# Optimization experiments

Hardware: AMD Instinct MI355X
Metric: run time of the kernel (lower is better)

The kernel has to match this reference:

```python
import jax, jax.numpy as jnp
import numpy as np

B, T, D = 4, 2048, 1024

def setup_inputs() -> dict:
    key = jax.random.key(0)
    kx, kq, kk, kv = jax.random.split(key, 4)
    scale = 1.0 / np.sqrt(D)
    return {
        "x": jax.random.normal(kx, (B, T, D), dtype=jnp.float32),
        "Wq": jax.random.normal(kq, (D, D), dtype=jnp.float32) * scale,
        "Wk": jax.random.normal(kk, (D, D), dtype=jnp.float32) * scale,
        "Wv": jax.random.normal(kv, (D, D), dtype=jnp.float32) * scale,
    }

def reference(x, Wq, Wk, Wv):
    # torch Linear: y = x @ W.T (no bias, qkv_bias=False)
    q = jnp.einsum("btd,od->bto", x, Wq)
    k = jnp.einsum("btd,od->bto", x, Wk)
    v = jnp.einsum("btd,od->bto", x, Wv)
    scores = jnp.einsum("bqd,bkd->bqk", q, k)
    # NOTE: source uses non-in-place masked_fill whose result is discarded,
    # so NO causal mask is actually applied. Faithfully reproduced here.
    inv_sqrt_d = 1.0 / np.sqrt(k.shape[-1]).astype(np.float32)
    weights = jax.nn.softmax(scores * inv_sqrt_d, axis=-1)
    # dropout p=0.0 -> identity
    return jnp.einsum("bqk,bkd->bqd", weights, v)
```

## Files before the change

kernel.cpp:

```cpp
#include <hip/hip_runtime.h>
#include <hip/hip_bf16.h>
#include <hip/hip_fp16.h>
#include <type_traits>

typedef _Float16 f16;
typedef __attribute__((ext_vector_type(8))) _Float16 f16x8;
typedef __attribute__((ext_vector_type(4))) float floatx4;

#define B_ 4
#define T_ 2048
#define D_ 1024

#define XB_OFF   0ul
#define WB_OFF   16777216ul
#define QKV_OFF  23068672ul
#define S_OFF    73400320ul
#define VT_OFF   0ul

#define ASYNC16(gp, lp) \
    __builtin_amdgcn_global_load_lds((const __attribute__((address_space(1))) unsigned int*)(gp), \
                                     (__attribute__((address_space(3))) unsigned int*)(lp), 16, 0, 0)

template<int N> __device__ __forceinline__ void vmwait() {
    if constexpr (N == 0)      asm volatile("s_waitcnt vmcnt(0)" ::: "memory");
    else if constexpr (N == 4) asm volatile("s_waitcnt vmcnt(4)" ::: "memory");
    else if constexpr (N == 6) asm volatile("s_waitcnt vmcnt(6)" ::: "memory");
    else static_assert(N == 0, "unsupported vmcnt literal");
}

__global__ __launch_bounds__(256) void cast_all(
    const float* __restrict__ x, const float* __restrict__ wq,
    const float* __restrict__ wk, const float* __restrict__ wv,
    f16* __restrict__ xb, f16* __restrict__ wb)
{
    long i = (long)blockIdx.x * 256 + threadIdx.x;
    const float4* src; f16* dst;
    if (i < 2097152L)            { src = (const float4*)x;  dst = xb; }
    else if (i < 2359296L)       { i -= 2097152L; src = (const float4*)wq; dst = wb; }
    else if (i < 2621440L)       { i -= 2359296L; src = (const float4*)wk; dst = wb + 1048576; }
    else                         { i -= 2621440L; src = (const float4*)wv; dst = wb + 2097152; }
    float4 v = src[i];
    union { f16 h[4]; uint2 u; } o;
    o.h[0] = (f16)v.x; o.h[1] = (f16)v.y; o.h[2] = (f16)v.z; o.h[3] = (f16)v.w;
    ((uint2*)dst)[i] = o.u;
}

template <typename CT, int BN, int WN>
__global__ __launch_bounds__(256, 3) void gemm_nt(
    const f16* __restrict__ A, int lda, long sA,
    const f16* __restrict__ B, int ldb, long sB,
    CT* __restrict__ C, int ldc, long sC,
    int K, float alpha)
{
    __shared__ f16 As[3][128 * 32];
    __shared__ f16 Bs[3][BN * 32];
    constexpr int L = 2 + BN / 64;

    const int tid = threadIdx.x;
    const int m0 = blockIdx.y * 128;
    const int n0 = blockIdx.x * BN;
    const int bz = blockIdx.z;
    A += (long)bz * sA;
    B += (long)bz * sB;
    C += (long)bz * sC;

    const int w  = tid >> 6;
    const int l  = tid & 63;
    const int wm = (w >> 1) * 64;
    const int wn = (w & 1) * WN;
    const int lr = l & 15;
    const int kg = l >> 4;
    const int kx = kg ^ ((lr >> 1) & 3);

    constexpr int NI = WN / 16;
    floatx4 acc[4][NI] = {};

    const int srow = tid >> 2;
    const int gsl  = (tid & 3) ^ ((tid >> 3) & 3);
    const long ldaL = lda, ldbL = ldb;
    const f16* Aptr = A + (long)(m0 + srow) * ldaL + gsl * 8;
    const f16* Bptr = B + (long)(n0 + srow) * ldbL + gsl * 8;

    auto stage = [&](f16* Ad, f16* Bd, int kk) {
        #pragma unroll
        for (int rh = 0; rh < 2; rh++)
            ASYNC16(Aptr + kk + rh * 64 * ldaL, Ad + rh * 2048 + w * 512);
        #pragma unroll
        for (int rh = 0; rh < BN / 64; rh++)
            ASYNC16(Bptr + kk + rh * 64 * ldbL, Bd + rh * 2048 + w * 512);
    };

    f16 *a0 = As[0], *a1 = As[1], *a2 = As[2];
    f16 *b0 = Bs[0], *b1 = Bs[1], *b2 = Bs[2];

    const int NT = K >> 5;
    stage(a0, b0, 0);
    stage(a1, b1, 32);

    for (int t = 0; t < NT; ++t) {
        if (t < NT - 1) vmwait<L>(); else vmwait<0>();
        __builtin_amdgcn_s_barrier();
        __builtin_amdgcn_sched_barrier(0);

        if (t + 2 < NT) stage(a2, b2, (t + 2) << 5);

        f16x8 af[4], bf[NI];
        #pragma unroll
        for (int mi = 0; mi < 4; mi++)
            af[mi] = *(const f16x8*)&a0[(wm + mi * 16 + lr) * 32 + kx * 8];
        #pragma unroll
        for (int ni = 0; ni < NI; ni++)
            bf[ni] = *(const f16x8*)&b0[(wn + ni * 16 + lr) * 32 + kx * 8];
        #pragma unroll
        for (int mi = 0; mi < 4; mi++)
            #pragma unroll
            for (int ni = 0; ni < NI; ni++)
                acc[mi][ni] = __builtin_amdgcn_mfma_f32_16x16x32_f16(af[mi], bf[ni], acc[mi][ni], 0, 0, 0);

        f16* ta = a0; a0 = a1; a1 = a2; a2 = ta;
        f16* tb = b0; b0 = b1; b1 = b2; b2 = tb;
    }

    #pragma unroll
    for (int mi = 0; mi < 4; mi++) {
        #pragma unroll
        for (int ni = 0; ni < NI; ni++) {
            #pragma unroll
            for (int r = 0; r < 4; r++) {
                int row = m0 + wm + mi * 16 + kg * 4 + r;
                int col = n0 + wn + ni * 16 + lr;
                float v = acc[mi][ni][r] * alpha;
                if constexpr (std::is_same<CT, float>::value)
                    C[(long)row * ldc + col] = v;
                else
                    C[(long)row * ldc + col] = (f16)v;
            }
        }
    }
}

__global__ __launch_bounds__(256) void transpose_v(const f16* __restrict__ qkv, f16* __restrict__ vt)
{
    __shared__ f16 tile[32][33];
    int b  = blockIdx.z;
    int j0 = blockIdx.x * 32;
    int d0 = blockIdx.y * 32;
    int tx = threadIdx.x & 31;
    int ty = threadIdx.x >> 5;
    #pragma unroll
    for (int i = 0; i < 4; i++) {
        int j = j0 + ty + i * 8;
        tile[ty + i * 8][tx] = qkv[((long)b * T_ + j) * 3072 + 2048 + d0 + tx];
    }
    __syncthreads();
    #pragma unroll
    for (int i = 0; i < 4; i++) {
        int d = d0 + ty + i * 8;
        vt[((long)b * D_ + d) * T_ + j0 + tx] = tile[tx][ty + i * 8];
    }
}

__global__ __launch_bounds__(256) void softmax_rows(f16* __restrict__ S)
{
    long row = (long)blockIdx.x * 4 + (threadIdx.x >> 6);
    int l = threadIdx.x & 63;
    uint4* p4 = (uint4*)(S + row * 2048);
    union U { uint4 u; f16 h[8]; } d[4];
    float v[32];
    float mx = -1e30f;
    #pragma unroll
    for (int i = 0; i < 4; i++) {
        d[i].u = p4[i * 64 + l];
        #pragma unroll
        for (int j = 0; j < 8; j++) { v[i * 8 + j] = (float)d[i].h[j]; mx = fmaxf(mx, v[i * 8 + j]); }
    }
    #pragma unroll
    for (int off = 32; off; off >>= 1) mx = fmaxf(mx, __shfl_xor(mx, off, 64));
    float s = 0.f;
    #pragma unroll
    for (int i = 0; i < 32; i++) { v[i] = __expf(v[i] - mx); s += v[i]; }
    #pragma unroll
    for (int off = 32; off; off >>= 1) s += __shfl_xor(s, off, 64);
    float inv = 1.f / s;
    #pragma unroll
    for (int i = 0; i < 4; i++) {
        #pragma unroll
        for (int j = 0; j < 8; j++) d[i].h[j] = (f16)(v[i * 8 + j] * inv);
        p4[i * 64 + l] = d[i].u;
    }
}

extern "C" void kernel_launch(void* const* d_in, const int* in_sizes, int n_in,
                              void* d_out, int out_size, void* d_ws, size_t ws_size,
                              hipStream_t stream)
{
    const float* x  = (const float*)d_in[0];
    const float* wq = (const float*)d_in[1];
    const float* wk = (const float*)d_in[2];
    const float* wv = (const float*)d_in[3];
    float* out = (float*)d_out;
    char* ws = (char*)d_ws;
    f16* xb  = (f16*)(ws + XB_OFF);
    f16* wb  = (f16*)(ws + WB_OFF);
    f16* qkv = (f16*)(ws + QKV_OFF);
    f16* s   = (f16*)(ws + S_OFF);
    f16* vt  = (f16*)(ws + VT_OFF);

    cast_all<<<11264, 256, 0, stream>>>(x, wq, wk, wv, xb, wb);

    gemm_nt<f16, 128, 64><<<dim3(24, 64, 1), 256, 0, stream>>>(
        xb, 1024, 0L, wb, 1024, 0L, qkv, 3072, 0L, 1024, 1.0f);

    transpose_v<<<dim3(64, 32, 4), 256, 0, stream>>>(qkv, vt);

    gemm_nt<f16, 128, 64><<<dim3(16, 16, 4), 256, 0, stream>>>(
        qkv,        3072, (long)T_ * 3072,
        qkv + 1024, 3072, (long)T_ * 3072,
        s,          2048, (long)T_ * 2048, 1024, 0.03125f);

    softmax_rows<<<2048, 256, 0, stream>>>(s);

    gemm_nt<float, 128, 64><<<dim3(8, 16, 4), 256, 0, stream>>>(
        s,  2048, (long)T_ * 2048,
        vt, 2048, (long)D_ * 2048,
        out, 1024, (long)T_ * 1024, 2048, 1.0f);
}
```

Baseline: 286.1 us.

## Add 256x256-tile 8-wave GEMM with split-phase pipelining for QKV and scores

Adds a new GEMM kernel that uses 512 threads and 256x256 output tiles with a K-step of 64. It double-buffers in LDS and interleaves LDS fragment reads, async global-to-LDS loads, barriers and MFMA bursts raised with s_setprio, in the style of ping-pong scheduling. The QKV projection and the QK^T score GEMM now use this kernel, while the PV GEMM keeps the old one. The larger tiles should increase data reuse and overlap memory traffic with math. In exchange the kernel carries heavy register pressure (128 accumulator floats) and launches fewer blocks: 384 and 256 workgroups for 256 CUs, which risks load imbalance.

```diff
diff --git a/kernel.cpp b/kernel.cpp
--- a/kernel.cpp
+++ b/kernel.cpp
@@ -27,6 +27,7 @@
     else if constexpr (N == 6) asm volatile("s_waitcnt vmcnt(6)" ::: "memory");
     else static_assert(N == 0, "unsupported vmcnt literal");
 }
+#define BAR()  do { __builtin_amdgcn_s_barrier(); __builtin_amdgcn_sched_barrier(0); } while (0)
 
 __global__ __launch_bounds__(256) void cast_all(
     const float* __restrict__ x, const float* __restrict__ wq,
@@ -43,6 +44,154 @@
     union { f16 h[4]; uint2 u; } o;
     o.h[0] = (f16)v.x; o.h[1] = (f16)v.y; o.h[2] = (f16)v.z; o.h[3] = (f16)v.w;
     ((uint2*)dst)[i] = o.u;
+}
+
+template <typename CT>
+__global__ __launch_bounds__(512, 2) void gemm8_nt(
+    const f16* __restrict__ A, int lda, long sA,
+    const f16* __restrict__ B, int ldb, long sB,
+    CT* __restrict__ C, int ldc, long sC,
+    int K, float alpha)
+{
+    __shared__ f16 lds[2][32768];
+
+    const int tid = threadIdx.x;
+    const int m0 = blockIdx.y * 256;
+    const int n0 = blockIdx.x * 256;
+    const int bz = blockIdx.z;
+    A += (long)bz * sA; B += (long)bz * sB; C += (long)bz * sC;
+
+    const int w  = tid >> 6;
+    const int l  = tid & 63;
+    const int wm = w >> 2;
+    const int wn = w & 3;
+    const int lr = l & 15;
+    const int kg = l >> 4;
+    const int kx = kg ^ ((lr >> 1) & 3);
+
+    floatx4 acc[8][4] = {};
+
+    const int srow = tid >> 2;
+    const int gsl  = (tid & 3) ^ ((tid >> 3) & 3);
+    const long ldaL = lda, ldbL = ldb;
+    const f16* Ag = A + (long)(m0 + srow) * ldaL + gsl * 8;
+    const f16* Bg = B + (long)(n0 + srow) * ldbL + gsl * 8;
+
+    auto stA = [&](int buf, int h, int t) {
+        f16* d = &lds[buf][h * 8192 + w * 512];
+        const f16* g = Ag + (long)(h * 128) * ldaL + t * 64;
+        ASYNC16(g,      d);
+        ASYNC16(g + 32, d + 4096);
+    };
+    auto stB = [&](int buf, int h, int t) {
+        f16* d = &lds[buf][16384 + h * 8192 + w * 512];
+        const f16* g = Bg + (long)(h * 128) * ldbL + t * 64;
+        ASYNC16(g,      d);
+        ASYNC16(g + 32, d + 4096);
+    };
+
+    const int NT = K >> 6;
+    stA(0, 0, 0); stA(0, 1, 0); stB(0, 0, 0); stB(0, 1, 0);
+    stB(1, 0, 1); stB(1, 1, 1);
+    vmwait<4>();
+    BAR();
+
+    const int abase = wm * 8192;
+    const int bbase = 16384 + (wn >> 1) * 8192 + (wn & 1) * 2048;
+    f16x8 af[2][4], bf0[2][2], bf1[2][2];
+
+    for (int u = 0; u < NT; ++u) {
+        const int cur = u & 1;
+        const f16* Lc = lds[cur];
+
+        #pragma unroll
+        for (int kk = 0; kk < 2; kk++) {
+            #pragma unroll
+            for (int mi = 0; mi < 4; mi++)
+                af[kk][mi] = *(const f16x8*)&Lc[abase + kk * 4096 + (mi * 16 + lr) * 32 + kx * 8];
+            #pragma unroll
+            for (int ni = 0; ni < 2; ni++)
+                bf0[kk][ni] = *(const f16x8*)&Lc[bbase + kk * 4096 + (ni * 16 + lr) * 32 + kx * 8];
+        }
+        if (u + 1 < NT) stA(cur ^ 1, 0, u + 1);
+        BAR();
+        __builtin_amdgcn_s_setprio(1);
+        #pragma unroll
+        for (int kk = 0; kk < 2; kk++)
+            #pragma unroll
+            for (int mi = 0; mi < 4; mi++)
+                #pragma unroll
+                for (int ni = 0; ni < 2; ni++)
+                    acc[mi][ni] = __builtin_amdgcn_mfma_f32_16x16x32_f16(af[kk][mi], bf0[kk][ni], acc[mi][ni], 0, 0, 0);
+        __builtin_amdgcn_s_setprio(0);
+        BAR();
+
+        #pragma unroll
+        for (int kk = 0; kk < 2; kk++)
+            #pragma unroll
+            for (int ni = 0; ni < 2; ni++)
+                bf1[kk][ni] = *(const f16x8*)&Lc[bbase + kk * 4096 + ((ni + 2) * 16 + lr) * 32 + kx * 8];
+        if (u + 1 < NT) stA(cur ^ 1, 1, u + 1);
+        BAR();
+        __builtin_amdgcn_s_setprio(1);
+        #pragma unroll
+        for (int kk = 0; kk < 2; kk++)
+            #pragma unroll
+            for (int mi = 0; mi < 4; mi++)
+                #pragma unroll
+                for (int ni = 0; ni < 2; ni++)
+                    acc[mi][ni + 2] = __builtin_amdgcn_mfma_f32_16x16x32_f16(af[kk][mi], bf1[kk][ni], acc[mi][ni + 2], 0, 0, 0);
+        __builtin_amdgcn_s_setprio(0);
+        BAR();
+
+        #pragma unroll
+        for (int kk = 0; kk < 2; kk++)
+            #pragma unroll
+            for (int mi = 0; mi < 4; mi++)
+                af[kk][mi] = *(const f16x8*)&Lc[abase + kk * 4096 + ((mi + 4) * 16 + lr) * 32 + kx * 8];
+        if (u + 2 < NT) stB(cur, 0, u + 2);
+        BAR();
+        __builtin_amdgcn_s_setprio(1);
+        #pragma unroll
+        for (int kk = 0; kk < 2; kk++)
+            #pragma unroll
+            for (int mi = 0; mi < 4; mi++)
+                #pragma unroll
+                for (int ni = 0; ni < 2; ni++)
+                    acc[mi + 4][ni + 2] = __builtin_amdgcn_mfma_f32_16x16x32_f16(af[kk][mi], bf1[kk][ni], acc[mi + 4][ni + 2], 0, 0, 0);
+        __builtin_amdgcn_s_setprio(0);
+        BAR();
+
+        if (u + 2 < NT) stB(cur, 1, u + 2);
+        BAR();
+        __builtin_amdgcn_s_setprio(1);
+        #pragma unroll
+        for (int kk = 0; kk < 2; kk++)
+            #pragma unroll
+            for (int mi = 0; mi < 4; mi++)
+                #pragma unroll
+                for (int ni = 0; ni < 2; ni++)
+                    acc[mi + 4][ni] = __builtin_amdgcn_mfma_f32_16x16x32_f16(af[kk][mi], bf0[kk][ni], acc[mi + 4][ni], 0, 0, 0);
+        __builtin_amdgcn_s_setprio(0);
+        if (u + 2 < NT)      vmwait<4>();
+        else if (u + 1 < NT) vmwait<0>();
+        BAR();
+    }
+
+    #pragma unroll
+    for (int mi = 0; mi < 8; mi++)
+        #pragma unroll
+        for (int ni = 0; ni < 4; ni++)
+            #pragma unroll
+            for (int r = 0; r < 4; r++) {
+                int row = m0 + wm * 128 + mi * 16 + kg * 4 + r;
+                int col = n0 + wn * 64 + ni * 16 + lr;
+                float v = acc[mi][ni][r] * alpha;
+                if constexpr (std::is_same<CT, float>::value)
+                    C[(long)row * ldc + col] = v;
+                else
+                    C[(long)row * ldc + col] = (f16)v;
+            }
 }
 
 template <typename CT, int BN, int WN>
@@ -208,12 +357,12 @@
 
     cast_all<<<11264, 256, 0, stream>>>(x, wq, wk, wv, xb, wb);
 
-    gemm_nt<f16, 128, 64><<<dim3(24, 64, 1), 256, 0, stream>>>(
+    gemm8_nt<f16><<<dim3(12, 32, 1), 512, 0, stream>>>(
         xb, 1024, 0L, wb, 1024, 0L, qkv, 3072, 0L, 1024, 1.0f);
 
     transpose_v<<<dim3(64, 32, 4), 256, 0, stream>>>(qkv, vt);
 
-    gemm_nt<f16, 128, 64><<<dim3(16, 16, 4), 256, 0, stream>>>(
+    gemm8_nt<f16><<<dim3(8, 8, 4), 512, 0, stream>>>(
         qkv,        3072, (long)T_ * 3072,
         qkv + 1024, 3072, (long)T_ * 3072,
         s,          2048, (long)T_ * 2048, 1024, 0.03125f);
```

New measurement: 264.6 us. 1.08x faster.
